# Performance work log

Hardware: AMD Instinct MI355X
Metric: run time of the kernel (lower is better)

Reference implementation:

```python
import jax, jax.numpy as jnp
from jax import lax
import numpy as np

D_MODEL, D_STATE, D_CONV, EXPAND = 192, 16, 3, 2
D_INNER = EXPAND * D_MODEL
B_, H_, W_ = 8, 128, 128
PAD = (D_CONV - 1) // 2
EPS = 1e-5


def setup_inputs() -> dict:
    key = jax.random.key(0)
    ks = jax.random.split(key, 8)
    s = 0.02
    return {
        "x": jax.random.normal(ks[0], (B_, D_MODEL, H_, W_), jnp.float32),
        "w_in": jax.random.normal(ks[1], (D_MODEL, 2 * D_INNER), jnp.float32) * s,
        "w_conv": jax.random.normal(ks[2], (D_INNER, 1, D_CONV, D_CONV), jnp.float32) * s,
        "b_conv": jnp.zeros((D_INNER,), jnp.float32),
        "w_x": jax.random.normal(ks[3], (D_INNER, 2 * D_STATE), jnp.float32) * s,
        "w_dt": jax.random.normal(ks[4], (D_STATE, D_INNER), jnp.float32) * s,
        "b_dt": jnp.zeros((D_INNER,), jnp.float32),
        "D_skip": jnp.ones((D_INNER,), jnp.float32),
        "w_out": jax.random.normal(ks[5], (D_INNER, D_MODEL), jnp.float32) * s,
        "gamma": jnp.ones((D_INNER,), jnp.float32),
        "beta": jnp.zeros((D_INNER,), jnp.float32),
    }


def _ss2d(x, w_in, w_conv, b_conv, w_x, w_dt, b_dt, D_skip, w_out, gamma, beta):
    B, C, H, W = x.shape
    L = H * W
    # NOTE: faithful to torch: x.reshape(B, H*W, C) on an NCHW tensor is a raw
    # row-major reinterpretation (same semantics as jnp.reshape), not a transpose.
    x_flat = x.reshape(B, L, C)
    x_proj = x_flat @ w_in                     # [B, L, 2*d_inner]
    x_inner, z = jnp.split(x_proj, 2, axis=-1)
    # depthwise conv over spatial dims
    xc = jnp.transpose(x_inner, (0, 2, 1)).reshape(B, D_INNER, H, W)
    xc = lax.conv_general_dilated(
        xc, w_conv, window_strides=(1, 1), padding=[(PAD, PAD), (PAD, PAD)],
        dimension_numbers=("NCHW", "OIHW", "NCHW"), feature_group_count=D_INNER,
    ) + b_conv[None, :, None, None]
    xc = jax.nn.silu(xc)
    xc = jnp.transpose(xc.reshape(B, D_INNER, L), (0, 2, 1))   # [B, L, d_inner]
    x_ssm = xc @ w_x                                            # [B, L, 2*d_state]
    B_ssm, C_ssm = jnp.split(x_ssm, 2, axis=-1)
    dt = jax.nn.softplus(B_ssm @ w_dt + b_dt)                   # [B, L, d_inner]
    # Original: deltaB = dt[...,None]*B_ssm[:,:,None,:]; einsum('blid,bld->bli', deltaB, C_ssm)
    # == dt * sum_d(B_ssm*C_ssm)  (deltaA is computed but never used -> dropped)
    bc = jnp.sum(B_ssm * C_ssm, axis=-1, keepdims=True)         # [B, L, 1]
    y = dt * bc + xc * D_skip                                   # [B, L, d_inner]
    y = y * jax.nn.silu(z)
    mu = jnp.mean(y, axis=-1, keepdims=True)
    var = jnp.mean(jnp.square(y - mu), axis=-1, keepdims=True)
    y = (y - mu) * lax.rsqrt(var + EPS) * gamma + beta
    out = y @ w_out                                             # [B, L, d_model]
    return jnp.transpose(out, (0, 2, 1)).reshape(B, C, H, W)


def reference(x, w_in, w_conv, b_conv, w_x, w_dt, b_dt, D_skip, w_out, gamma, beta):
    return _ss2d(x, w_in, w_conv, b_conv, w_x, w_dt, b_dt, D_skip, w_out, gamma, beta)
```

## Files before the change

### kernel.cpp

```cpp
#include <hip/hip_runtime.h>
#include <hip/hip_bf16.h>

typedef __bf16 bf16x8 __attribute__((ext_vector_type(8)));
typedef __bf16 bf16x4 __attribute__((ext_vector_type(4)));
typedef float  f32x4  __attribute__((ext_vector_type(4)));

__device__ __forceinline__ f32x4 mfma16(bf16x8 a, bf16x8 b, f32x4 c) {
    return __builtin_amdgcn_mfma_f32_16x16x32_bf16(a, b, c, 0, 0, 0);
}
__device__ __forceinline__ float silu_f(float v) { return v / (1.f + __expf(-v)); }
__device__ __forceinline__ float softplus_fast(float v) {
    float r = __logf(1.f + __expf(v));
    return v > 15.f ? v : r;
}

#define CC 192
#define DI 384
#define LL 16384
#define HH 128
#define WW 128
#define LTOT 131072L


__global__ void k0_prep(const float* __restrict__ w_in, const float* __restrict__ w_x,
                        const float* __restrict__ w_dt, const float* __restrict__ w_out,
                        __bf16* __restrict__ wt_in, __bf16* __restrict__ wt_x,
                        __bf16* __restrict__ wt_dt, __bf16* __restrict__ wt_out) {
    int tid = blockIdx.x * blockDim.x + threadIdx.x;
    int nth = gridDim.x * blockDim.x;
    for (int i = tid; i < 768 * 192; i += nth) {
        int nf = i / 192, k = i % 192;
        int nc = nf >> 6, n = nf & 63;
        int e = (n * 192 + k) ^ ((n & 7) << 3);
        wt_in[nc * 12288 + e] = (__bf16)w_in[k * 768 + nf];
    }
    for (int i = tid; i < 32 * 384;  i += nth) { int n = i / 384, k = i % 384; wt_x[i]  = (__bf16)w_x[k * 32 + n]; }
    for (int i = tid; i < 384 * 16;  i += nth) { int ch = i / 16, k = i % 16;  wt_dt[i] = (__bf16)w_dt[k * 384 + ch]; }
    for (int i = tid; i < 192 * 384; i += nth) { int n = i / 384, k = i % 384; wt_out[i] = (__bf16)w_out[k * 192 + n]; }
}

__global__ __launch_bounds__(256, 2) void k1_proj(
        const float* __restrict__ x, const __bf16* __restrict__ wt_in,
        __bf16* __restrict__ xin, __bf16* __restrict__ zsb) {
    __shared__ __attribute__((aligned(16))) __bf16 Bs[2][12288];
    __shared__ __attribute__((aligned(16))) __bf16 bounce[4][32 * 68];
    const int tid = threadIdx.x;
    const int lane = tid & 63, wv = tid >> 6;
    const int lq = lane & 15, quad = lane >> 4;
    const long mbase = (long)blockIdx.x * 128;
    __bf16* bb = &bounce[wv][0];

    bf16x8 af[2][6];
#pragma unroll
    for (int mt = 0; mt < 2; mt++) {
        const float* xr = x + (mbase + wv * 32 + mt * 16 + lq) * CC;
#pragma unroll
        for (int ks = 0; ks < 6; ks++) {
            float4 v0 = *(const float4*)(xr + ks * 32 + quad * 8);
            float4 v1 = *(const float4*)(xr + ks * 32 + quad * 8 + 4);
            bf16x8 t;
            t[0] = (__bf16)v0.x; t[1] = (__bf16)v0.y; t[2] = (__bf16)v0.z; t[3] = (__bf16)v0.w;
            t[4] = (__bf16)v1.x; t[5] = (__bf16)v1.y; t[6] = (__bf16)v1.z; t[7] = (__bf16)v1.w;
            af[mt][ks] = t;
        }
    }

    auto stage = [&](int b, int nc) {
        const char* src = (const char*)(wt_in + nc * 12288);
        char* dst = (char*)&Bs[b][0];
#pragma unroll
        for (int i = 0; i < 6; i++) {
            int off = (wv * 6 + i) * 1024;
            __builtin_amdgcn_global_load_lds(
                (const __attribute__((address_space(1))) void*)(src + off + lane * 16),
                (__attribute__((address_space(3))) void*)(dst + off),
                16, 0, 0);
        }
    };

    stage(0, 0);
    __syncthreads();

    int buf = 0;
    for (int nc = 0; nc < 12; nc++) {
        if (nc < 11) stage(buf ^ 1, nc + 1);

        f32x4 A0[4], A1[4];
#pragma unroll
        for (int nt = 0; nt < 4; nt++) {
            A0[nt] = (f32x4){0.f, 0.f, 0.f, 0.f};
            A1[nt] = (f32x4){0.f, 0.f, 0.f, 0.f};
#pragma unroll
            for (int ks = 0; ks < 6; ks++) {
                const int row = nt * 16 + lq;
                const int e = (row * 192 + ks * 32 + quad * 8) ^ ((lq & 7) << 3);
                bf16x8 bf = *(const bf16x8*)(&Bs[buf][e]);
                A0[nt] = mfma16(af[0][ks], bf, A0[nt]);
                A1[nt] = mfma16(af[1][ks], bf, A1[nt]);
            }
        }
        const bool isz = (nc >= 6);
#pragma unroll
        for (int nt = 0; nt < 4; nt++) {
#pragma unroll
            for (int r = 0; r < 4; r++) {
                float v0 = A0[nt][r], v1 = A1[nt][r];
                if (isz) { v0 = silu_f(v0); v1 = silu_f(v1); }
                bb[(quad * 4 + r) * 68 + nt * 16 + lq] = (__bf16)v0;
                bb[(16 + quad * 4 + r) * 68 + nt * 16 + lq] = (__bf16)v1;
            }
        }
        __builtin_amdgcn_wave_barrier();
        __bf16* dst = isz ? zsb : xin;
        const long chunk = isz ? nc - 6 : nc;
#pragma unroll
        for (int k = 0; k < 4; k++) {
            int u = lane + k * 64;
            int row = u >> 3, c8 = u & 7;
            unsigned long long lo = *(const unsigned long long*)(&bb[row * 68 + c8 * 8]);
            unsigned long long hi = *(const unsigned long long*)(&bb[row * 68 + c8 * 8 + 4]);
            ulonglong2 val; val.x = lo; val.y = hi;
            *(ulonglong2*)(dst + (chunk * LTOT + mbase + wv * 32 + row) * 64 + c8 * 8) = val;
        }
        __syncthreads();
        buf ^= 1;
    }
}

__global__ __launch_bounds__(256, 4) void k3_ssm(
        const __bf16* __restrict__ xin, const __bf16* __restrict__ zsb,
        const __bf16* __restrict__ wtx, const __bf16* __restrict__ wtdt,
        const __bf16* __restrict__ wtout, const float* __restrict__ wconv,
        const float* __restrict__ bconv, const float* __restrict__ bdt,
        const float* __restrict__ dskip, const float* __restrict__ gamma,
        const float* __restrict__ beta, float* __restrict__ out) {
    __shared__ __attribute__((aligned(16))) __bf16 xcb[32 * 392];
    __shared__ __attribute__((aligned(16))) char region1[15360];
    float* wcvs = (float*)region1;
    float* bcvs = (float*)(region1 + 13824);
    float* Bf   = (float*)region1;
    float* Cf   = (float*)(region1 + 2560);
    __bf16* dts = (__bf16*)region1;
    float* bcarr = (float*)(region1 + 12800);

    const int tid = threadIdx.x;
    const int lane = tid & 63, wv = tid >> 6;
    const int lq = lane & 15, quad = lane >> 4;
    const int t0g = blockIdx.x * 32;

    const int te = tid >> 3, part = tid & 7;
    const long tok = t0g + te;

    bf16x8 zpre[6];
#pragma unroll
    for (int h = 0; h < 2; h++)
#pragma unroll
        for (int g = 0; g < 3; g++) {
            const int chg = h * 192 + part * 24 + g * 8;
            zpre[h * 3 + g] = *(const bf16x8*)(zsb + ((long)(chg >> 6) * LTOT + tok) * 64 + (chg & 63));
        }

    for (int u = tid; u < 9 * 384; u += 256) { int ch = u / 9, tap = u % 9; wcvs[tap * 384 + ch] = wconv[u]; }
    for (int u = tid; u < 384; u += 256) bcvs[u] = bconv[u];
    __syncthreads();

    const int hblk = (t0g & (LL - 1)) >> 7;
    const int w0 = t0g & 127;
#pragma unroll
    for (int k = 0; k < 6; k++) {
        int u = tid + k * 256;
        int t = u / 48, c8 = u % 48;
        long tk = t0g + t;
        const long cbase = (long)(c8 >> 3) * LTOT;
        const int coff = (c8 & 7) * 8;
        float acc[8];
        float4 b0 = *(const float4*)(bcvs + c8 * 8);
        float4 b1 = *(const float4*)(bcvs + c8 * 8 + 4);
        acc[0] = b0.x; acc[1] = b0.y; acc[2] = b0.z; acc[3] = b0.w;
        acc[4] = b1.x; acc[5] = b1.y; acc[6] = b1.z; acc[7] = b1.w;
#pragma unroll
        for (int dy = -1; dy <= 1; dy++) {
            int h2 = hblk + dy;
            if (h2 < 0 || h2 >= HH) continue;
#pragma unroll
            for (int dx = -1; dx <= 1; dx++) {
                int w2 = w0 + t + dx;
                if (w2 < 0 || w2 >= WW) continue;
                bf16x8 v = *(const bf16x8*)(xin + (cbase + tk + dy * WW + dx) * 64 + coff);
                const float* wp = &wcvs[((dy + 1) * 3 + (dx + 1)) * 384 + c8 * 8];
#pragma unroll
                for (int j = 0; j < 8; j++) acc[j] += (float)v[j] * wp[j];
            }
        }
        bf16x8 r;
#pragma unroll
        for (int j = 0; j < 8; j++) r[j] = (__bf16)silu_f(acc[j]);
        *(bf16x8*)(&xcb[t * 392 + c8 * 8]) = r;
    }
    __syncthreads();

    {
        const int wt = wv & 1, wsel = wv >> 1;
        f32x4 a4 = {0.f, 0.f, 0.f, 0.f};
#pragma unroll
        for (int ks = 0; ks < 12; ks++) {
            bf16x8 a = *(const bf16x8*)(&xcb[(wt * 16 + lq) * 392 + ks * 32 + quad * 8]);
            bf16x8 b = *(const bf16x8*)(wtx + (wsel * 16 + lq) * 384 + ks * 32 + quad * 8);
            a4 = mfma16(a, b, a4);
        }
        float* dstf = wsel ? Cf : Bf;
#pragma unroll
        for (int r = 0; r < 4; r++)
            dstf[(wt * 16 + quad * 4 + r) * 20 + lq] = a4[r];
    }
    __syncthreads();

    {
        int t = tid >> 3;
        int s0 = (tid & 7) * 2;
        float p = Bf[t * 20 + s0] * Cf[t * 20 + s0] + Bf[t * 20 + s0 + 1] * Cf[t * 20 + s0 + 1];
        p += __shfl_xor(p, 1, 64);
        p += __shfl_xor(p, 2, 64);
        p += __shfl_xor(p, 4, 64);
        if ((lane & 7) == 0) bcarr[t] = p;
    }
    bf16x8 zero8;
#pragma unroll
    for (int j = 0; j < 8; j++) zero8[j] = (__bf16)0.f;
    bf16x8 aA[2];
#pragma unroll
    for (int mt = 0; mt < 2; mt++) {
        if (quad < 2) {
            const float* bp = Bf + (mt * 16 + lq) * 20 + quad * 8;
            f32x4 lo = *(const f32x4*)(bp);
            f32x4 hi = *(const f32x4*)(bp + 4);
            bf16x8 t8;
            t8[0] = (__bf16)lo[0]; t8[1] = (__bf16)lo[1]; t8[2] = (__bf16)lo[2]; t8[3] = (__bf16)lo[3];
            t8[4] = (__bf16)hi[0]; t8[5] = (__bf16)hi[1]; t8[6] = (__bf16)hi[2]; t8[7] = (__bf16)hi[3];
            aA[mt] = t8;
        } else {
            aA[mt] = zero8;
        }
    }
    __syncthreads();

    float s1 = 0.f, s2 = 0.f;

#pragma unroll
    for (int h = 0; h < 2; h++) {
        f32x4 dacc[3][2];
        float bdtv[3];
#pragma unroll
        for (int j = 0; j < 3; j++) {
            int chg = h * 192 + (wv * 3 + j) * 16 + lq;
            bf16x8 bf = (quad < 2) ? *(const bf16x8*)(wtdt + (long)chg * 16 + quad * 8) : zero8;
            bdtv[j] = bdt[chg];
#pragma unroll
            for (int mt = 0; mt < 2; mt++) {
                f32x4 z4 = {0.f, 0.f, 0.f, 0.f};
                dacc[j][mt] = mfma16(aA[mt], bf, z4);
            }
        }
#pragma unroll
        for (int j = 0; j < 3; j++)
#pragma unroll
            for (int mt = 0; mt < 2; mt++)
#pragma unroll
                for (int r = 0; r < 4; r++)
                    dts[(mt * 16 + quad * 4 + r) * 200 + (wv * 3 + j) * 16 + lq] =
                        (__bf16)(dacc[j][mt][r] + bdtv[j]);
        __syncthreads();

#pragma unroll
        for (int g = 0; g < 3; g++) {
            const int chl = part * 24 + g * 8;
            const int chg = h * 192 + chl;
            bf16x8 d8 = *(const bf16x8*)(&dts[te * 200 + chl]);
            bf16x8 xc8 = *(const bf16x8*)(&xcb[te * 392 + chg]);
            bf16x8 z8 = zpre[h * 3 + g];
            float4 d0 = *(const float4*)(dskip + chg);
            float4 d1 = *(const float4*)(dskip + chg + 4);
            float ds[8] = {d0.x, d0.y, d0.z, d0.w, d1.x, d1.y, d1.z, d1.w};
            const float bcv = bcarr[te];
#pragma unroll
            for (int j = 0; j < 8; j++) {
                float dtv = softplus_fast((float)d8[j]);
                float yv = (dtv * bcv + (float)xc8[j] * ds[j]) * (float)z8[j];
                s1 += yv; s2 += yv * yv;
                xc8[j] = (__bf16)yv;
            }
            *(bf16x8*)(&xcb[te * 392 + chg]) = xc8;
        }
        __syncthreads();
    }

    {
        s1 += __shfl_xor(s1, 1, 64); s2 += __shfl_xor(s2, 1, 64);
        s1 += __shfl_xor(s1, 2, 64); s2 += __shfl_xor(s2, 2, 64);
        s1 += __shfl_xor(s1, 4, 64); s2 += __shfl_xor(s2, 4, 64);
        float mu = s1 * (1.f / 384.f);
        float var = s2 * (1.f / 384.f) - mu * mu;
        float rstd = rsqrtf(var + 1e-5f);
#pragma unroll
        for (int gg = 0; gg < 6; gg++) {
            const int h2 = gg / 3, g3 = gg % 3;
            const int ch = h2 * 192 + part * 24 + g3 * 8;
            bf16x8 v = *(const bf16x8*)(&xcb[te * 392 + ch]);
            float4 g0 = *(const float4*)(gamma + ch);
            float4 g1 = *(const float4*)(gamma + ch + 4);
            float4 be0 = *(const float4*)(beta + ch);
            float4 be1 = *(const float4*)(beta + ch + 4);
            float gm[8] = {g0.x, g0.y, g0.z, g0.w, g1.x, g1.y, g1.z, g1.w};
            float bt[8] = {be0.x, be0.y, be0.z, be0.w, be1.x, be1.y, be1.z, be1.w};
#pragma unroll
            for (int j = 0; j < 8; j++) v[j] = (__bf16)(((float)v[j] - mu) * rstd * gm[j] + bt[j]);
            *(bf16x8*)(&xcb[te * 392 + ch]) = v;
        }
    }
    __syncthreads();

    {
        const int bimg = t0g >> 14;
        const int l0 = t0g & (LL - 1);
        f32x4 acc[3][2];
#pragma unroll
        for (int j = 0; j < 3; j++)
#pragma unroll
            for (int mt = 0; mt < 2; mt++) acc[j][mt] = (f32x4){0.f, 0.f, 0.f, 0.f};
#pragma unroll
        for (int ks = 0; ks < 12; ks++) {
            bf16x8 bfr[3];
#pragma unroll
            for (int j = 0; j < 3; j++) {
                int c = (wv * 3 + j) * 16 + lq;
                bfr[j] = *(const bf16x8*)(wtout + (long)c * 384 + ks * 32 + quad * 8);
            }
#pragma unroll
            for (int mt = 0; mt < 2; mt++) {
                bf16x8 afr = *(const bf16x8*)(&xcb[(mt * 16 + lq) * 392 + ks * 32 + quad * 8]);
#pragma unroll
                for (int j = 0; j < 3; j++) acc[j][mt] = mfma16(afr, bfr[j], acc[j][mt]);
            }
        }
#pragma unroll
        for (int j = 0; j < 3; j++) {
            const int c = (wv * 3 + j) * 16 + lq;
#pragma unroll
            for (int mt = 0; mt < 2; mt++)
                *(f32x4*)(out + ((long)(bimg * CC + c)) * LL + l0 + mt * 16 + quad * 4) = acc[j][mt];
        }
    }
}

extern "C" void kernel_launch(void* const* d_in, const int* in_sizes, int n_in,
                              void* d_out, int out_size, void* d_ws, size_t ws_size,
                              hipStream_t stream) {
    (void)in_sizes; (void)n_in; (void)out_size; (void)ws_size;
    const float* x      = (const float*)d_in[0];
    const float* w_in   = (const float*)d_in[1];
    const float* w_conv = (const float*)d_in[2];
    const float* b_conv = (const float*)d_in[3];
    const float* w_x    = (const float*)d_in[4];
    const float* w_dt   = (const float*)d_in[5];
    const float* b_dt   = (const float*)d_in[6];
    const float* D_skip = (const float*)d_in[7];
    const float* w_out  = (const float*)d_in[8];
    const float* gamma  = (const float*)d_in[9];
    const float* beta   = (const float*)d_in[10];
    float* out = (float*)d_out;

    char* ws = (char*)d_ws;
    __bf16* wt_in  = (__bf16*)(ws);
    __bf16* wt_x   = (__bf16*)(ws + 294912);
    __bf16* wt_dt  = (__bf16*)(ws + 319488);
    __bf16* wt_out = (__bf16*)(ws + 331776);
    __bf16* xin    = (__bf16*)(ws + 479232);
    __bf16* zsb    = (__bf16*)(ws + 479232 + 100663296);

    k0_prep<<<96, 256, 0, stream>>>(w_in, w_x, w_dt, w_out, wt_in, wt_x, wt_dt, wt_out);
    k1_proj<<<1024, 256, 0, stream>>>(x, wt_in, xin, zsb);
    k3_ssm<<<4096, 256, 0, stream>>>(xin, zsb, wt_x, wt_dt, wt_out, w_conv, b_conv,
                                     b_dt, D_skip, gamma, beta, out);
}
```

Baseline: 468.3 us.

## Fuse z-gate projection into SSM kernel, drop z intermediate buffer

Moves the z-half of the input projection out of the projection kernel and recomputes it inside the SSM kernel from x with MFMA, applying SiLU there. This removes the global write and read of the bf16 z buffer (about 100 MB round trip). The projection kernel now handles only the x_inner half and reads weights directly from global memory instead of staging them through LDS, which allows higher occupancy. The cost is extra x reads and MFMA work in the SSM kernel, plus uncached weight loads from global memory.

```diff
diff --git a/kernel.cpp b/kernel.cpp
--- a/kernel.cpp
+++ b/kernel.cpp
@@ -28,27 +28,21 @@
                         __bf16* __restrict__ wt_dt, __bf16* __restrict__ wt_out) {
     int tid = blockIdx.x * blockDim.x + threadIdx.x;
     int nth = gridDim.x * blockDim.x;
-    for (int i = tid; i < 768 * 192; i += nth) {
-        int nf = i / 192, k = i % 192;
-        int nc = nf >> 6, n = nf & 63;
-        int e = (n * 192 + k) ^ ((n & 7) << 3);
-        wt_in[nc * 12288 + e] = (__bf16)w_in[k * 768 + nf];
-    }
+    for (int i = tid; i < 768 * 192; i += nth) { int n = i / 192, k = i % 192; wt_in[i] = (__bf16)w_in[k * 768 + n]; }
     for (int i = tid; i < 32 * 384;  i += nth) { int n = i / 384, k = i % 384; wt_x[i]  = (__bf16)w_x[k * 32 + n]; }
     for (int i = tid; i < 384 * 16;  i += nth) { int ch = i / 16, k = i % 16;  wt_dt[i] = (__bf16)w_dt[k * 384 + ch]; }
     for (int i = tid; i < 192 * 384; i += nth) { int n = i / 384, k = i % 384; wt_out[i] = (__bf16)w_out[k * 192 + n]; }
 }
 
-__global__ __launch_bounds__(256, 2) void k1_proj(
+__global__ __launch_bounds__(256, 4) void k1_proj(
         const float* __restrict__ x, const __bf16* __restrict__ wt_in,
-        __bf16* __restrict__ xin, __bf16* __restrict__ zsb) {
-    __shared__ __attribute__((aligned(16))) __bf16 Bs[2][12288];
-    __shared__ __attribute__((aligned(16))) __bf16 bounce[4][32 * 68];
+        __bf16* __restrict__ xin) {
+    __shared__ __attribute__((aligned(16))) __bf16 wb[4 * 2 * 32 * 68];
     const int tid = threadIdx.x;
     const int lane = tid & 63, wv = tid >> 6;
     const int lq = lane & 15, quad = lane >> 4;
     const long mbase = (long)blockIdx.x * 128;
-    __bf16* bb = &bounce[wv][0];
+    __bf16* wbase = wb + wv * (2 * 32 * 68);
 
     bf16x8 af[2][6];
 #pragma unroll
@@ -65,26 +59,7 @@
         }
     }
 
-    auto stage = [&](int b, int nc) {
-        const char* src = (const char*)(wt_in + nc * 12288);
-        char* dst = (char*)&Bs[b][0];
-#pragma unroll
-        for (int i = 0; i < 6; i++) {
-            int off = (wv * 6 + i) * 1024;
-            __builtin_amdgcn_global_load_lds(
-                (const __attribute__((address_space(1))) void*)(src + off + lane * 16),
-                (__attribute__((address_space(3))) void*)(dst + off),
-                16, 0, 0);
-        }
-    };
-
-    stage(0, 0);
-    __syncthreads();
-
-    int buf = 0;
-    for (int nc = 0; nc < 12; nc++) {
-        if (nc < 11) stage(buf ^ 1, nc + 1);
-
+    for (int nc = 0; nc < 6; nc++) {
         f32x4 A0[4], A1[4];
 #pragma unroll
         for (int nt = 0; nt < 4; nt++) {
@@ -92,27 +67,21 @@
             A1[nt] = (f32x4){0.f, 0.f, 0.f, 0.f};
 #pragma unroll
             for (int ks = 0; ks < 6; ks++) {
-                const int row = nt * 16 + lq;
-                const int e = (row * 192 + ks * 32 + quad * 8) ^ ((lq & 7) << 3);
-                bf16x8 bf = *(const bf16x8*)(&Bs[buf][e]);
+                bf16x8 bf = *(const bf16x8*)(wt_in + (long)(nc * 64 + nt * 16 + lq) * CC + ks * 32 + quad * 8);
                 A0[nt] = mfma16(af[0][ks], bf, A0[nt]);
                 A1[nt] = mfma16(af[1][ks], bf, A1[nt]);
             }
         }
-        const bool isz = (nc >= 6);
+        __bf16* bb = wbase + (nc & 1) * (32 * 68);
 #pragma unroll
         for (int nt = 0; nt < 4; nt++) {
 #pragma unroll
             for (int r = 0; r < 4; r++) {
-                float v0 = A0[nt][r], v1 = A1[nt][r];
-                if (isz) { v0 = silu_f(v0); v1 = silu_f(v1); }
-                bb[(quad * 4 + r) * 68 + nt * 16 + lq] = (__bf16)v0;
-                bb[(16 + quad * 4 + r) * 68 + nt * 16 + lq] = (__bf16)v1;
+                bb[(quad * 4 + r) * 68 + nt * 16 + lq] = (__bf16)A0[nt][r];
+                bb[(16 + quad * 4 + r) * 68 + nt * 16 + lq] = (__bf16)A1[nt][r];
             }
         }
         __builtin_amdgcn_wave_barrier();
-        __bf16* dst = isz ? zsb : xin;
-        const long chunk = isz ? nc - 6 : nc;
 #pragma unroll
         for (int k = 0; k < 4; k++) {
             int u = lane + k * 64;
@@ -120,15 +89,15 @@
             unsigned long long lo = *(const unsigned long long*)(&bb[row * 68 + c8 * 8]);
             unsigned long long hi = *(const unsigned long long*)(&bb[row * 68 + c8 * 8 + 4]);
             ulonglong2 val; val.x = lo; val.y = hi;
-            *(ulonglong2*)(dst + (chunk * LTOT + mbase + wv * 32 + row) * 64 + c8 * 8) = val;
-        }
-        __syncthreads();
-        buf ^= 1;
+            *(ulonglong2*)(xin + ((long)nc * LTOT + mbase + wv * 32 + row) * 64 + c8 * 8) = val;
+        }
+        __builtin_amdgcn_wave_barrier();
     }
 }
 
 __global__ __launch_bounds__(256, 4) void k3_ssm(
-        const __bf16* __restrict__ xin, const __bf16* __restrict__ zsb,
+        const float* __restrict__ x, const __bf16* __restrict__ xin,
+        const __bf16* __restrict__ wt_in,
         const __bf16* __restrict__ wtx, const __bf16* __restrict__ wtdt,
         const __bf16* __restrict__ wtout, const float* __restrict__ wconv,
         const float* __restrict__ bconv, const float* __restrict__ bdt,
@@ -151,17 +120,51 @@
     const int te = tid >> 3, part = tid & 7;
     const long tok = t0g + te;
 
-    bf16x8 zpre[6];
-#pragma unroll
-    for (int h = 0; h < 2; h++)
-#pragma unroll
-        for (int g = 0; g < 3; g++) {
-            const int chg = h * 192 + part * 24 + g * 8;
-            zpre[h * 3 + g] = *(const bf16x8*)(zsb + ((long)(chg >> 6) * LTOT + tok) * 64 + (chg & 63));
-        }
+    bf16x8 afz[2][6];
+#pragma unroll
+    for (int mt = 0; mt < 2; mt++) {
+        const float* xr = x + (long)(t0g + mt * 16 + lq) * CC;
+#pragma unroll
+        for (int ks = 0; ks < 6; ks++) {
+            float4 v0 = *(const float4*)(xr + ks * 32 + quad * 8);
+            float4 v1 = *(const float4*)(xr + ks * 32 + quad * 8 + 4);
+            bf16x8 t;
+            t[0] = (__bf16)v0.x; t[1] = (__bf16)v0.y; t[2] = (__bf16)v0.z; t[3] = (__bf16)v0.w;
+            t[4] = (__bf16)v1.x; t[5] = (__bf16)v1.y; t[6] = (__bf16)v1.z; t[7] = (__bf16)v1.w;
+            afz[mt][ks] = t;
+        }
+    }
+
+#pragma unroll
+    for (int h = 0; h < 2; h++) {
+#pragma unroll
+        for (int j = 0; j < 3; j++) {
+            f32x4 zac0 = {0.f, 0.f, 0.f, 0.f}, zac1 = {0.f, 0.f, 0.f, 0.f};
+            const int zch = h * 192 + (wv * 3 + j) * 16 + lq;
+#pragma unroll
+            for (int ks = 0; ks < 6; ks++) {
+                bf16x8 bf = *(const bf16x8*)(wt_in + (long)(384 + zch) * CC + ks * 32 + quad * 8);
+                zac0 = mfma16(afz[0][ks], bf, zac0);
+                zac1 = mfma16(afz[1][ks], bf, zac1);
+            }
+#pragma unroll
+            for (int r = 0; r < 4; r++) {
+                xcb[(quad * 4 + r) * 392 + zch] = (__bf16)silu_f(zac0[r]);
+                xcb[(16 + quad * 4 + r) * 392 + zch] = (__bf16)silu_f(zac1[r]);
+            }
+        }
+    }
 
     for (int u = tid; u < 9 * 384; u += 256) { int ch = u / 9, tap = u % 9; wcvs[tap * 384 + ch] = wconv[u]; }
     for (int u = tid; u < 384; u += 256) bcvs[u] = bconv[u];
+    __syncthreads();
+
+    bf16x8 zreg[6];
+#pragma unroll
+    for (int h = 0; h < 2; h++)
+#pragma unroll
+        for (int g = 0; g < 3; g++)
+            zreg[h * 3 + g] = *(const bf16x8*)(&xcb[te * 392 + h * 192 + part * 24 + g * 8]);
     __syncthreads();
 
     const int hblk = (t0g & (LL - 1)) >> 7;
@@ -277,7 +280,7 @@
             const int chg = h * 192 + chl;
             bf16x8 d8 = *(const bf16x8*)(&dts[te * 200 + chl]);
             bf16x8 xc8 = *(const bf16x8*)(&xcb[te * 392 + chg]);
-            bf16x8 z8 = zpre[h * 3 + g];
+            bf16x8 z8 = zreg[h * 3 + g];
             float4 d0 = *(const float4*)(dskip + chg);
             float4 d1 = *(const float4*)(dskip + chg + 4);
             float ds[8] = {d0.x, d0.y, d0.z, d0.w, d1.x, d1.y, d1.z, d1.w};
@@ -375,10 +378,9 @@
     __bf16* wt_dt  = (__bf16*)(ws + 319488);
     __bf16* wt_out = (__bf16*)(ws + 331776);
     __bf16* xin    = (__bf16*)(ws + 479232);
-    __bf16* zsb    = (__bf16*)(ws + 479232 + 100663296);
 
     k0_prep<<<96, 256, 0, stream>>>(w_in, w_x, w_dt, w_out, wt_in, wt_x, wt_dt, wt_out);
-    k1_proj<<<1024, 256, 0, stream>>>(x, wt_in, xin, zsb);
-    k3_ssm<<<4096, 256, 0, stream>>>(xin, zsb, wt_x, wt_dt, wt_out, w_conv, b_conv,
+    k1_proj<<<1024, 256, 0, stream>>>(x, wt_in, xin);
+    k3_ssm<<<4096, 256, 0, stream>>>(x, xin, wt_in, wt_x, wt_dt, wt_out, w_conv, b_conv,
                                      b_dt, D_skip, gamma, beta, out);
 }
```

New measurement: 546.6 us. +16.7%, slower.

## Read projection and conv weights directly from global instead of staging in LDS

Applied to the files above, without the earlier changes.

The input projection kernel drops its double-buffered LDS staging of w_in (global_load_lds with swizzle) and the per-iteration block barriers. It reads B fragments straight from global/L2 and uses double-buffered per-wave bounce buffers with only wave barriers, which shrinks LDS and raises occupancy to 4 blocks. The SSM kernel stops staging the conv weights and bias in LDS and reads a pre-transposed copy (made in the prep kernel) from global with float4 loads, removing a block barrier. The tradeoff is more global/L2 traffic, and uncoalesced B-fragment loads, in place of LDS reuse.

```diff
diff --git a/kernel.cpp b/kernel.cpp
--- a/kernel.cpp
+++ b/kernel.cpp
@@ -24,31 +24,28 @@
 
 __global__ void k0_prep(const float* __restrict__ w_in, const float* __restrict__ w_x,
                         const float* __restrict__ w_dt, const float* __restrict__ w_out,
+                        const float* __restrict__ w_conv,
                         __bf16* __restrict__ wt_in, __bf16* __restrict__ wt_x,
-                        __bf16* __restrict__ wt_dt, __bf16* __restrict__ wt_out) {
+                        __bf16* __restrict__ wt_dt, __bf16* __restrict__ wt_out,
+                        float* __restrict__ wcv_t) {
     int tid = blockIdx.x * blockDim.x + threadIdx.x;
     int nth = gridDim.x * blockDim.x;
-    for (int i = tid; i < 768 * 192; i += nth) {
-        int nf = i / 192, k = i % 192;
-        int nc = nf >> 6, n = nf & 63;
-        int e = (n * 192 + k) ^ ((n & 7) << 3);
-        wt_in[nc * 12288 + e] = (__bf16)w_in[k * 768 + nf];
-    }
+    for (int i = tid; i < 768 * 192; i += nth) { int n = i / 192, k = i % 192; wt_in[i] = (__bf16)w_in[k * 768 + n]; }
     for (int i = tid; i < 32 * 384;  i += nth) { int n = i / 384, k = i % 384; wt_x[i]  = (__bf16)w_x[k * 32 + n]; }
     for (int i = tid; i < 384 * 16;  i += nth) { int ch = i / 16, k = i % 16;  wt_dt[i] = (__bf16)w_dt[k * 384 + ch]; }
     for (int i = tid; i < 192 * 384; i += nth) { int n = i / 384, k = i % 384; wt_out[i] = (__bf16)w_out[k * 192 + n]; }
-}
-
-__global__ __launch_bounds__(256, 2) void k1_proj(
+    for (int i = tid; i < 9 * 384;   i += nth) { int tap = i / 384, ch = i % 384; wcv_t[i] = w_conv[ch * 9 + tap]; }
+}
+
+__global__ __launch_bounds__(256, 4) void k1_proj(
         const float* __restrict__ x, const __bf16* __restrict__ wt_in,
         __bf16* __restrict__ xin, __bf16* __restrict__ zsb) {
-    __shared__ __attribute__((aligned(16))) __bf16 Bs[2][12288];
-    __shared__ __attribute__((aligned(16))) __bf16 bounce[4][32 * 68];
+    __shared__ __attribute__((aligned(16))) __bf16 wb[4 * 2 * 32 * 68];
     const int tid = threadIdx.x;
     const int lane = tid & 63, wv = tid >> 6;
     const int lq = lane & 15, quad = lane >> 4;
     const long mbase = (long)blockIdx.x * 128;
-    __bf16* bb = &bounce[wv][0];
+    __bf16* wbase = wb + wv * (2 * 32 * 68);
 
     bf16x8 af[2][6];
 #pragma unroll
@@ -65,26 +62,7 @@
         }
     }
 
-    auto stage = [&](int b, int nc) {
-        const char* src = (const char*)(wt_in + nc * 12288);
-        char* dst = (char*)&Bs[b][0];
-#pragma unroll
-        for (int i = 0; i < 6; i++) {
-            int off = (wv * 6 + i) * 1024;
-            __builtin_amdgcn_global_load_lds(
-                (const __attribute__((address_space(1))) void*)(src + off + lane * 16),
-                (__attribute__((address_space(3))) void*)(dst + off),
-                16, 0, 0);
-        }
-    };
-
-    stage(0, 0);
-    __syncthreads();
-
-    int buf = 0;
     for (int nc = 0; nc < 12; nc++) {
-        if (nc < 11) stage(buf ^ 1, nc + 1);
-
         f32x4 A0[4], A1[4];
 #pragma unroll
         for (int nt = 0; nt < 4; nt++) {
@@ -92,14 +70,13 @@
             A1[nt] = (f32x4){0.f, 0.f, 0.f, 0.f};
 #pragma unroll
             for (int ks = 0; ks < 6; ks++) {
-                const int row = nt * 16 + lq;
-                const int e = (row * 192 + ks * 32 + quad * 8) ^ ((lq & 7) << 3);
-                bf16x8 bf = *(const bf16x8*)(&Bs[buf][e]);
+                bf16x8 bf = *(const bf16x8*)(wt_in + (long)(nc * 64 + nt * 16 + lq) * CC + ks * 32 + quad * 8);
                 A0[nt] = mfma16(af[0][ks], bf, A0[nt]);
                 A1[nt] = mfma16(af[1][ks], bf, A1[nt]);
             }
         }
         const bool isz = (nc >= 6);
+        __bf16* bb = wbase + (nc & 1) * (32 * 68);
 #pragma unroll
         for (int nt = 0; nt < 4; nt++) {
 #pragma unroll
@@ -122,22 +99,19 @@
             ulonglong2 val; val.x = lo; val.y = hi;
             *(ulonglong2*)(dst + (chunk * LTOT + mbase + wv * 32 + row) * 64 + c8 * 8) = val;
         }
-        __syncthreads();
-        buf ^= 1;
+        __builtin_amdgcn_wave_barrier();
     }
 }
 
 __global__ __launch_bounds__(256, 4) void k3_ssm(
         const __bf16* __restrict__ xin, const __bf16* __restrict__ zsb,
         const __bf16* __restrict__ wtx, const __bf16* __restrict__ wtdt,
-        const __bf16* __restrict__ wtout, const float* __restrict__ wconv,
+        const __bf16* __restrict__ wtout, const float* __restrict__ wcv_t,
         const float* __restrict__ bconv, const float* __restrict__ bdt,
         const float* __restrict__ dskip, const float* __restrict__ gamma,
         const float* __restrict__ beta, float* __restrict__ out) {
     __shared__ __attribute__((aligned(16))) __bf16 xcb[32 * 392];
     __shared__ __attribute__((aligned(16))) char region1[15360];
-    float* wcvs = (float*)region1;
-    float* bcvs = (float*)(region1 + 13824);
     float* Bf   = (float*)region1;
     float* Cf   = (float*)(region1 + 2560);
     __bf16* dts = (__bf16*)region1;
@@ -159,10 +133,6 @@
             const int chg = h * 192 + part * 24 + g * 8;
             zpre[h * 3 + g] = *(const bf16x8*)(zsb + ((long)(chg >> 6) * LTOT + tok) * 64 + (chg & 63));
         }
-
-    for (int u = tid; u < 9 * 384; u += 256) { int ch = u / 9, tap = u % 9; wcvs[tap * 384 + ch] = wconv[u]; }
-    for (int u = tid; u < 384; u += 256) bcvs[u] = bconv[u];
-    __syncthreads();
 
     const int hblk = (t0g & (LL - 1)) >> 7;
     const int w0 = t0g & 127;
@@ -174,8 +144,8 @@
         const long cbase = (long)(c8 >> 3) * LTOT;
         const int coff = (c8 & 7) * 8;
         float acc[8];
-        float4 b0 = *(const float4*)(bcvs + c8 * 8);
-        float4 b1 = *(const float4*)(bcvs + c8 * 8 + 4);
+        float4 b0 = *(const float4*)(bconv + c8 * 8);
+        float4 b1 = *(const float4*)(bconv + c8 * 8 + 4);
         acc[0] = b0.x; acc[1] = b0.y; acc[2] = b0.z; acc[3] = b0.w;
         acc[4] = b1.x; acc[5] = b1.y; acc[6] = b1.z; acc[7] = b1.w;
 #pragma unroll
@@ -187,9 +157,12 @@
                 int w2 = w0 + t + dx;
                 if (w2 < 0 || w2 >= WW) continue;
                 bf16x8 v = *(const bf16x8*)(xin + (cbase + tk + dy * WW + dx) * 64 + coff);
-                const float* wp = &wcvs[((dy + 1) * 3 + (dx + 1)) * 384 + c8 * 8];
-#pragma unroll
-                for (int j = 0; j < 8; j++) acc[j] += (float)v[j] * wp[j];
+                const float* wp = wcv_t + ((dy + 1) * 3 + (dx + 1)) * 384 + c8 * 8;
+                float4 w0v = *(const float4*)(wp);
+                float4 w1v = *(const float4*)(wp + 4);
+                float wf[8] = {w0v.x, w0v.y, w0v.z, w0v.w, w1v.x, w1v.y, w1v.z, w1v.w};
+#pragma unroll
+                for (int j = 0; j < 8; j++) acc[j] += (float)v[j] * wf[j];
             }
         }
         bf16x8 r;
@@ -374,11 +347,13 @@
     __bf16* wt_x   = (__bf16*)(ws + 294912);
     __bf16* wt_dt  = (__bf16*)(ws + 319488);
     __bf16* wt_out = (__bf16*)(ws + 331776);
-    __bf16* xin    = (__bf16*)(ws + 479232);
-    __bf16* zsb    = (__bf16*)(ws + 479232 + 100663296);
-
-    k0_prep<<<96, 256, 0, stream>>>(w_in, w_x, w_dt, w_out, wt_in, wt_x, wt_dt, wt_out);
+    float*  wcv_t  = (float*)(ws + 479232);
+    __bf16* xin    = (__bf16*)(ws + 493056);
+    __bf16* zsb    = (__bf16*)(ws + 493056 + 100663296);
+
+    k0_prep<<<96, 256, 0, stream>>>(w_in, w_x, w_dt, w_out, w_conv,
+                                    wt_in, wt_x, wt_dt, wt_out, wcv_t);
     k1_proj<<<1024, 256, 0, stream>>>(x, wt_in, xin, zsb);
-    k3_ssm<<<4096, 256, 0, stream>>>(xin, zsb, wt_x, wt_dt, wt_out, w_conv, b_conv,
+    k3_ssm<<<4096, 256, 0, stream>>>(xin, zsb, wt_x, wt_dt, wt_out, wcv_t, b_conv,
                                      b_dt, D_skip, gamma, beta, out);
 }
```

After: 550.1 us. 1.17x slower.
